# Kernel optimization log

Hardware: AMD Instinct MI355X
Metric: run time of the kernel (lower is better)

Reference implementation:

```python
import jax, jax.numpy as jnp
import numpy as np

B, T, I, H, N_LAYERS = 32, 1024, 512, 512, 4


def _custom_lstm(x, w, u, b):
    # x: [B,T,I]; w: [4,I,H] (gate order i,f,c,o); u: [4,H,H]; b: [4,H]
    # Preactivations for all timesteps/gates at once: [T,4,B,H]
    pre = jnp.einsum('bti,gih->tgbh', x, w) + b[None, :, None, :]
    h0 = jnp.zeros((x.shape[0], b.shape[-1]), x.dtype)
    c0 = jnp.zeros_like(h0)

    def step(carry, p):
        h, c = carry
        rec = jnp.einsum('bh,ghk->gbk', h, u)
        g = jax.nn.sigmoid(p + rec)          # all 4 gates use sigmoid (incl. g_t, as in source)
        i_t, f_t, g_t, o_t = g[0], g[1], g[2], g[3]
        c = f_t + c + i_t * g_t              # faithful: additive, not f*c
        h = o_t + jnp.tanh(c)                # faithful: additive, not o*tanh(c)
        return (h, c), h

    (h, c), hs = jax.lax.scan(step, (h0, c0), pre)
    return h, c, jnp.transpose(hs, (1, 0, 2))  # [B,T,H]


def _vlstm(x, h_prev, wx, wh, u, b):
    # x: [B,T,I]; h_prev: [B,T,H]; wx: [4,I,H]; wh: [4,H,H]; u: [4,H,H]; b: [4,H]
    # Source bug preserved: ALL gates use u[0] (u_i) and b[0] (b_i).
    pre = (jnp.einsum('bti,gih->tgbh', x, wx)
           + jnp.einsum('bth,ghk->tgbk', h_prev, wh)
           + b[0][None, None, None, :])
    u_i = u[0]
    h0 = jnp.zeros((x.shape[0], b.shape[-1]), x.dtype)
    c0 = jnp.zeros_like(h0)

    def step(carry, p):
        h, c = carry
        rec = h @ u_i                        # shared recurrent term for all gates
        g = jax.nn.sigmoid(p + rec[None])
        i_t, f_t, g_t, o_t = g[0], g[1], g[2], g[3]
        c = f_t + c + i_t * g_t
        h = o_t + jnp.tanh(c)
        return (h, c), h

    (h, c), hs = jax.lax.scan(step, (h0, c0), pre)
    return h, c, jnp.transpose(hs, (1, 0, 2))


def setup_inputs() -> dict:
    key = jax.random.key(0)
    ks = jax.random.split(key, 6)
    stdv = 1.0 / np.sqrt(H)
    u_ = lambda k, shp: jax.random.uniform(k, shp, jnp.float32, -stdv, stdv)
    L = N_LAYERS - 1
    return {
        'x': jax.random.normal(ks[0], (B, T, I), jnp.float32),
        'w1': u_(ks[1], (4, I, H)),
        'u1': u_(ks[2], (4, H, H)),
        'b1': u_(ks[3], (4, H)),
        'wx': u_(ks[4], (L, 4, I, H)),
        'wh': u_(ks[5], (L, 4, H, H)),
        'uv': u_(jax.random.fold_in(key, 10), (L, 4, H, H)),
        'bv': u_(jax.random.fold_in(key, 11), (L, 4, H)),
    }


def reference(x, w1, u1, b1, wx, wh, uv, bv):
    h_t, c_t, h_vec = _custom_lstm(x, w1, u1, b1)
    for l in range(wx.shape[0]):  # verbose path: each VLSTM sees raw x + prev layer h_vec
        h_t, c_t, h_vec = _vlstm(x, h_vec, wx[l], wh[l], uv[l], bv[l])
    return h_t, c_t, h_vec
```

## Files before the change

### kernel.cpp

```cpp
#include <hip/hip_runtime.h>

typedef unsigned short u16;
typedef unsigned int u32;
typedef unsigned long long u64;
typedef __attribute__((ext_vector_type(4))) float f32x4;
typedef __attribute__((ext_vector_type(8))) short short8;
typedef __attribute__((ext_vector_type(4))) short short4v;

__device__ __forceinline__ float bf2f(u16 v){ u32 b = ((u32)v)<<16; float f; __builtin_memcpy(&f,&b,4); return f; }
__device__ __forceinline__ u16 f2bf(float f){ u32 b; __builtin_memcpy(&b,&f,4); b = b + 0x7fffu + ((b>>16)&1u); return (u16)(b>>16); }
__device__ __forceinline__ float sigm(float x){ return 1.f/(1.f+__expf(-x)); }
__device__ __forceinline__ float tanh_a(float x){ return 1.f - 2.f/(__expf(2.f*x)+1.f); }
__device__ __forceinline__ int imin(int a, int b){ return a<b?a:b; }

typedef const __attribute__((address_space(1))) u32* gas1;
typedef __attribute__((address_space(3))) u32* las3;
__device__ __forceinline__ void gld16(const u16* g, u16* l){
  __builtin_amdgcn_global_load_lds((gas1)g, (las3)l, 16, 0, 0);
}

__device__ __forceinline__ void pub64(u32* p, u64 v){
  __hip_atomic_store((u64*)p, v, __ATOMIC_RELAXED, __HIP_MEMORY_SCOPE_AGENT);
}
__device__ __forceinline__ void pub32(u32* p, u32 v){
  __hip_atomic_store(p, v, __ATOMIC_RELAXED, __HIP_MEMORY_SCOPE_AGENT);
}
__device__ __forceinline__ u64 pol64(const u32* p){
  return __hip_atomic_load((const u64*)p, __ATOMIC_RELAXED, __HIP_MEMORY_SCOPE_AGENT);
}
__device__ __forceinline__ u32 pol32(const u32* p){
  return __hip_atomic_load(p, __ATOMIC_RELAXED, __HIP_MEMORY_SCOPE_AGENT);
}

__global__ void cast_x_kernel(const float* __restrict__ in, u16* __restrict__ out){
  int i = blockIdx.x*256 + threadIdx.x;
  for (; i < 4194304; i += 2048*256){
    f32x4 v = ((const f32x4*)in)[i];
    int e = i*4;
    int b = e >> 19, t = (e >> 9) & 1023, k = e & 511;
    short4v o;
    o[0]=(short)f2bf(v[0]); o[1]=(short)f2bf(v[1]); o[2]=(short)f2bf(v[2]); o[3]=(short)f2bf(v[3]);
    *(short4v*)&out[(size_t)(t*32+b)*512 + k] = o;
  }
}

__global__ void pack_w_kernel(const float* __restrict__ w1, const float* __restrict__ wx, const float* __restrict__ wh,
                              u16* __restrict__ w1p, u16* __restrict__ wxwhp){
  int e = blockIdx.x*256 + threadIdx.x;
  for (; e < 7340032; e += 2048*256){
    if (e < 1048576){
      int h = e & 511, k = (e>>9)&511, g = e>>18;
      w1p[(size_t)(g*512+h)*512 + k] = f2bf(w1[(size_t)g*262144 + (size_t)k*512 + h]);
    } else {
      int r = e - 1048576;
      int lv = r >> 21;
      int q = r & 2097151;
      int n = q >> 10, k = q & 1023;
      int g = n >> 9, h = n & 511;
      float v;
      if (k < 512) v = wx[(size_t)lv*1048576 + (size_t)g*262144 + (size_t)k*512 + h];
      else         v = wh[(size_t)lv*1048576 + (size_t)g*262144 + (size_t)(k-512)*512 + h];
      wxwhp[(size_t)lv*2097152 + (size_t)n*1024 + k] = f2bf(v);
    }
  }
}

__global__ void cast_u_kernel(const float* __restrict__ u1, const float* __restrict__ uv,
                              u16* __restrict__ u1p, u16* __restrict__ uv0p){
  int e = blockIdx.x*256 + threadIdx.x;
  for (; e < 1835008; e += 1024*256){
    if (e < 1048576) u1p[e] = f2bf(u1[e]);
    else { int r = e - 1048576; uv0p[r] = f2bf(uv[(size_t)(r>>18)*1048576 + (r & 262143)]); }
  }
}

__global__ __launch_bounds__(256) void gemm_pre_kernel(
    const u16* __restrict__ A1, const u16* __restrict__ B1,
    const float* __restrict__ bias, int bmask,
    u16* __restrict__ Out)
{
  __shared__ u16 As[128*64];
  __shared__ u16 Bs[128*64];
  const int tid = threadIdx.x;
  const int w = tid>>6, lane = tid&63;
  const int l15 = lane&15, l4 = lane>>4;
  const int m0 = blockIdx.x*128, n0 = blockIdx.y*128;
  const int wm = w>>1, wn = w&1;
  f32x4 acc[4][4];
#pragma unroll
  for (int a=0;a<4;a++)
#pragma unroll
    for (int bq=0;bq<4;bq++) acc[a][bq] = (f32x4){0.f,0.f,0.f,0.f};

  for (int kt=0;kt<8;kt++){
    const int k0 = kt*64;
    __syncthreads();
#pragma unroll
    for (int i=0;i<4;i++){
      int chunk = w*4 + i;
      int fb = chunk*1024 + lane*16;
      int row = fb>>7;
      int slot = (fb>>4)&7;
      const u16* srcA = A1 + (size_t)(m0+row)*512 + k0 + ((slot ^ (row&7))<<3);
      gld16(srcA, (u16*)As + chunk*512);
      const u16* srcB = B1 + (size_t)(n0+row)*512 + k0 + ((slot ^ (row&7))<<3);
      gld16(srcB, (u16*)Bs + chunk*512);
    }
    __syncthreads();
#pragma unroll
    for (int kk=0;kk<2;kk++){
      short8 af[4], bfq[4];
#pragma unroll
      for (int mi=0;mi<4;mi++){
        int row = wm*64 + mi*16 + l15;
        int s16 = l4 + kk*4;
        af[mi] = *(const short8*)&As[row*64 + ((s16 ^ (row&7))<<3)];
      }
#pragma unroll
      for (int ni=0;ni<4;ni++){
        int row = wn*64 + ni*16 + l15;
        int s16 = l4 + kk*4;
        bfq[ni] = *(const short8*)&Bs[row*64 + ((s16 ^ (row&7))<<3)];
      }
#pragma unroll
      for (int mi=0;mi<4;mi++)
#pragma unroll
        for (int ni=0;ni<4;ni++)
          acc[mi][ni] = __builtin_amdgcn_mfma_f32_16x16x32_bf16(af[mi], bfq[ni], acc[mi][ni], 0,0,0);
    }
  }
#pragma unroll
  for (int ni=0;ni<4;ni++){
    int col = n0 + wn*64 + ni*16 + l15;
    float bb = bias[col & bmask];
#pragma unroll
    for (int mi=0;mi<4;mi++){
#pragma unroll
      for (int i=0;i<4;i++){
        int row = m0 + wm*64 + mi*16 + l4*4 + i;
        Out[(size_t)row*2048 + col] = f2bf(acc[mi][ni][i] + bb);
      }
    }
  }
}

__global__ __launch_bounds__(512,2) void mega_kernel(
    const u16* __restrict__ pre1, const u16* __restrict__ u1p,
    const u16* __restrict__ uv0p, const u16* __restrict__ xb,
    const u16* __restrict__ wxwhp, const float* __restrict__ bv,
    u32* hring, u32* pring, u32* prog, float* __restrict__ out)
{
  __shared__ char smem[33024];
  const int bid = blockIdx.x;
  const int tid = threadIdx.x;
  const int lane = tid&63, w = tid>>6;
  const int l15 = lane&15, l4 = lane>>4;

  if (bid < 16){
    u16* hs = (u16*)smem;
    float* recb = (float*)(smem+16384);
    const int gk = bid & 7, gb = bid >> 3;
    const int b0 = gb*16, kb = gk*64;
    const int g = w>>1, ch = w&1;
    short8 bfr[2][16];
#pragma unroll
    for (int n=0;n<2;n++){
      const u16* up = u1p + (size_t)g*262144 + (kb + ch*32 + n*16 + l15);
#pragma unroll
      for (int s=0;s<16;s++){
        int kbase = s*32 + l4*8;
#pragma unroll
        for (int j=0;j<8;j++) bfr[n][s][j] = (short)up[(size_t)(kbase+j)*512];
      }
    }
    { short8 z = {0,0,0,0,0,0,0,0};
      for (int i=tid;i<1024;i+=512) ((short8*)hs)[i]=z; }
    const int b = tid>>5, q = tid&31;
    const int hc2 = q*2;
    float cA=0.f, cB=0.f;
    __syncthreads();

    for (int t=0;t<1024;++t){
      if ((t&15)==0 && t>=32){
        int thr = t-32;
        for(;;){
          int m0=(int)pol32(&prog[0]); m0=imin(m0,(int)pol32(&prog[1]));
          m0=imin(m0,(int)pol32(&prog[2])); m0=imin(m0,(int)pol32(&prog[3]));
          if (m0>=thr) break;
          __builtin_amdgcn_s_sleep(8);
        }
      }
      const u16* prow = pre1 + ((size_t)(t*32 + b0 + b))*2048 + kb + hc2;
      u32 pw0 = *(const u32*)(prow);
      u32 pw1 = *(const u32*)(prow+512);
      u32 pw2 = *(const u32*)(prow+1024);
      u32 pw3 = *(const u32*)(prow+1536);
      f32x4 acc0 = {0.f,0.f,0.f,0.f}, acc1 = {0.f,0.f,0.f,0.f};
      {
        int rb = l15*512, sw = (l15&7)<<3;
#pragma unroll
        for (int s=0;s<16;s++){
          short8 a = *(const short8*)&hs[rb + ((s*32 + l4*8) ^ sw)];
          acc0 = __builtin_amdgcn_mfma_f32_16x16x32_bf16(a, bfr[0][s], acc0, 0,0,0);
          acc1 = __builtin_amdgcn_mfma_f32_16x16x32_bf16(a, bfr[1][s], acc1, 0,0,0);
        }
      }
      {
        int base = g*64 + ch*32 + l15;
#pragma unroll
        for (int i=0;i<4;i++){
          recb[(l4*4+i)*256 + base]      = acc0[i];
          recb[(l4*4+i)*256 + base + 16] = acc1[i];
        }
      }
      __syncthreads();
      float ri0 = recb[b*256 + hc2],       ri1 = recb[b*256 + hc2+1];
      float rf0 = recb[b*256 + 64 + hc2],  rf1 = recb[b*256 + 64 + hc2+1];
      float rg0 = recb[b*256 + 128 + hc2], rg1 = recb[b*256 + 128 + hc2+1];
      float ro0 = recb[b*256 + 192 + hc2], ro1 = recb[b*256 + 192 + hc2+1];
      float gi0 = sigm(bf2f((u16)(pw0&0xffffu)) + ri0), gi1 = sigm(bf2f((u16)(pw0>>16)) + ri1);
      float gf0 = sigm(bf2f((u16)(pw1&0xffffu)) + rf0), gf1 = sigm(bf2f((u16)(pw1>>16)) + rf1);
      float gg0 = sigm(bf2f((u16)(pw2&0xffffu)) + rg0), gg1 = sigm(bf2f((u16)(pw2>>16)) + rg1);
      float go0 = sigm(bf2f((u16)(pw3&0xffffu)) + ro0), go1 = sigm(bf2f((u16)(pw3>>16)) + ro1);
      cA = gf0 + cA + gi0*gg0; float h0v = go0 + tanh_a(cA);
      cB = gf1 + cB + gi1*gg1; float h1v = go1 + tanh_a(cB);
      u16 hb0 = f2bf(h0v), hb1 = f2bf(h1v);
      const u32 tag = (u32)(t+1);
      u32* slot = hring + (size_t)(t&63)*16384;
      u64 msg = (((u64)((tag<<16)|(u32)hb1))<<32) | (u64)((tag<<16)|(u32)hb0);
      pub64(&slot[(size_t)(b0+b)*512 + kb + hc2], msg);
      u32 hpair = (u32)hb0 | ((u32)hb1<<16);
      *(u32*)&hs[b*512 + ((kb+hc2) ^ ((b&7)<<3))] = hpair;
      {
        const u32* srcg = slot + (size_t)(b0+b)*512;
        u64 nv[7];
        for(;;){
#pragma unroll
          for (int j=0;j<7;j++){
            int fc = q*14 + 2*j;
            int ac = fc + (fc>=kb ? 64 : 0);
            nv[j] = pol64(&srcg[ac]);
          }
          u32 ok = 1;
#pragma unroll
          for (int j=0;j<7;j++){
            if ((u32)(((u32)nv[j])>>16) != tag) ok=0;
            if ((u32)(nv[j]>>48) != tag) ok=0;
          }
          if (ok) break;
          __builtin_amdgcn_s_sleep(1);
        }
#pragma unroll
        for (int j=0;j<7;j++){
          int fc = q*14 + 2*j;
          int ac = fc + (fc>=kb ? 64 : 0);
          u32 pair = ((u32)nv[j]&0xffffu) | ((u32)((nv[j]>>32)&0xffffu)<<16);
          *(u32*)&hs[b*512 + (ac ^ ((b&7)<<3))] = pair;
        }
      }
      __syncthreads();
      if (tid==0) pub32(&prog[32+bid], (u32)(t+1));
    }
  } else if (bid < 28){
    u16* hs = (u16*)smem;
    float* recb = (float*)(smem+16384);
    const int l = 1 + ((bid-16)>>2);
    const int lv = l-1;
    const int sub = (bid-16)&3;
    const int ch = sub&1, gb = sub>>1;
    const int b0 = gb*16, cbase = ch*256;
    short8 bfr[2][16];
#pragma unroll
    for (int n=0;n<2;n++){
      const u16* up = uv0p + (size_t)lv*262144 + (cbase + w*32 + n*16 + l15);
#pragma unroll
      for (int s=0;s<16;s++){
        int kbase = s*32 + l4*8;
#pragma unroll
        for (int j=0;j<8;j++) bfr[n][s][j] = (short)up[(size_t)(kbase+j)*512];
      }
    }
    { short8 z = {0,0,0,0,0,0,0,0};
      for (int i=tid;i<1024;i+=512) ((short8*)hs)[i]=z; }
    const int b = tid>>5, q = tid&31;
    const int oc = cbase + q*8;
    float cv[8];
#pragma unroll
    for (int j=0;j<8;j++) cv[j]=0.f;
    u32* hr = hring + (size_t)l*1048576;
    u32* pr = pring + (size_t)lv*4194304;
    const int is_last = (l==3);
    __syncthreads();

    for (int t=0;t<1024;++t){
      const u32 tag = (u32)(t+1);
      if (l<3 && (t&15)==0 && t>=32){
        int thr=t-32;
        const int pbase = l*4;
        for(;;){
          int m0=(int)pol32(&prog[pbase]); m0=imin(m0,(int)pol32(&prog[pbase+1]));
          m0=imin(m0,(int)pol32(&prog[pbase+2])); m0=imin(m0,(int)pol32(&prog[pbase+3]));
          if (m0>=thr) break;
          __builtin_amdgcn_s_sleep(8);
        }
      }
      const u32* ps = pr + (size_t)(t&63)*65536 + (size_t)(b0+b)*2048;
      u64 pv[16];
#pragma unroll
      for (int gq=0;gq<4;gq++)
#pragma unroll
        for (int j=0;j<4;j++)
          pv[gq*4+j] = pol64(&ps[gq*512 + oc + 2*j]);
      f32x4 acc0={0.f,0.f,0.f,0.f}, acc1={0.f,0.f,0.f,0.f};
      {
        int rb=l15*512, sw=(l15&7)<<3;
#pragma unroll
        for (int s=0;s<16;s++){
          short8 a = *(const short8*)&hs[rb + ((s*32+l4*8)^sw)];
          acc0 = __builtin_amdgcn_mfma_f32_16x16x32_bf16(a, bfr[0][s], acc0, 0,0,0);
          acc1 = __builtin_amdgcn_mfma_f32_16x16x32_bf16(a, bfr[1][s], acc1, 0,0,0);
        }
      }
      {
        int base = w*32 + l15;
#pragma unroll
        for (int i=0;i<4;i++){
          recb[(l4*4+i)*256 + base]    = acc0[i];
          recb[(l4*4+i)*256 + base+16] = acc1[i];
        }
      }
      for(;;){
        u32 ok=1;
#pragma unroll
        for (int i=0;i<16;i++){
          if ((u32)(((u32)pv[i])>>16) != tag) ok=0;
          if ((u32)(pv[i]>>48) != tag) ok=0;
        }
        if (ok) break;
        for(;;){
          int mn = 0x7fffffff;
#pragma unroll
          for (int g=0; g<4; g++){
            int cg0 = g*4 + ch*2;
            mn = imin(mn, (int)pol32(&prog[64 + lv*32 + (cg0*2+gb)]));
            mn = imin(mn, (int)pol32(&prog[64 + lv*32 + ((cg0+1)*2+gb)]));
          }
          if (mn >= (int)tag) break;
          __builtin_amdgcn_s_sleep(4);
        }
#pragma unroll
        for (int gq=0;gq<4;gq++)
#pragma unroll
          for (int j=0;j<4;j++)
            pv[gq*4+j] = pol64(&ps[gq*512 + oc + 2*j]);
      }
      __syncthreads();
      short8 hvv; float hf[8]; u32 msgw[8];
#pragma unroll
      for (int j=0;j<8;j++){
        float r = recb[b*256 + q*8 + j];
        int wi = j>>1;
        u32 w0 = (j&1) ? (u32)(pv[wi]>>32)    : (u32)pv[wi];
        u32 w1v= (j&1) ? (u32)(pv[4+wi]>>32)  : (u32)pv[4+wi];
        u32 w2 = (j&1) ? (u32)(pv[8+wi]>>32)  : (u32)pv[8+wi];
        u32 w3 = (j&1) ? (u32)(pv[12+wi]>>32) : (u32)pv[12+wi];
        float gi = sigm(bf2f((u16)(w0&0xffffu)) + r);
        float gf = sigm(bf2f((u16)(w1v&0xffffu)) + r);
        float gg = sigm(bf2f((u16)(w2&0xffffu)) + r);
        float go = sigm(bf2f((u16)(w3&0xffffu)) + r);
        cv[j] = gf + cv[j] + gi*gg;
        float h = go + tanh_a(cv[j]);
        u16 hb = f2bf(h);
        hvv[j]=(short)hb; hf[j]=h; msgw[j] = (tag<<16)|(u32)hb;
      }
      u32* hslot = hr + (size_t)(t&63)*16384 + (size_t)(b0+b)*512;
#pragma unroll
      for (int j=0;j<4;j++){
        u64 m = (((u64)msgw[2*j+1])<<32) | (u64)msgw[2*j];
        pub64(&hslot[oc + 2*j], m);
      }
      *(short8*)&hs[b*512 + (oc ^ ((b&7)<<3))] = hvv;
      if (is_last){
        f32x4 h4a={hf[0],hf[1],hf[2],hf[3]}, h4b={hf[4],hf[5],hf[6],hf[7]};
        *(f32x4*)&out[32768 + ((size_t)((b0+b)*1024+t))*512 + oc]   = h4a;
        *(f32x4*)&out[32768 + ((size_t)((b0+b)*1024+t))*512 + oc+4] = h4b;
        if (t==1023){
          *(f32x4*)&out[(size_t)(b0+b)*512 + oc]   = h4a;
          *(f32x4*)&out[(size_t)(b0+b)*512 + oc+4] = h4b;
          f32x4 c4a={cv[0],cv[1],cv[2],cv[3]}, c4b={cv[4],cv[5],cv[6],cv[7]};
          *(f32x4*)&out[16384 + (size_t)(b0+b)*512 + oc]   = c4a;
          *(f32x4*)&out[16384 + (size_t)(b0+b)*512 + oc+4] = c4b;
        }
      }
      {
        const u32* src = hslot + (ch^1)*256 + q*8;
        u64 nv[4];
        for(;;){
#pragma unroll
          for (int j=0;j<4;j++) nv[j] = pol64(&src[2*j]);
          u32 ok=1;
#pragma unroll
          for (int j=0;j<4;j++){
            if ((u32)(((u32)nv[j])>>16)!=tag) ok=0;
            if ((u32)(nv[j]>>48)!=tag) ok=0;
          }
          if (ok) break;
          __builtin_amdgcn_s_sleep(1);
        }
        short8 hh;
#pragma unroll
        for (int j=0;j<4;j++){
          hh[2*j]   = (short)(u16)(nv[j] & 0xffffu);
          hh[2*j+1] = (short)(u16)((nv[j]>>32) & 0xffffu);
        }
        int pc = (ch^1)*256 + q*8;
        *(short8*)&hs[b*512 + (pc ^ ((b&7)<<3))] = hh;
      }
      __syncthreads();
      if (tid==0) pub32(&prog[(l-1)*4 + sub], (u32)(t+1));
    }
  } else {
    u16* hstage = (u16*)smem;
    const int idx = bid - 28;
    const int lv = idx >> 5;
    const int r  = idx & 31;
    const int gb = r & 1, cg = r >> 1;
    const int b0 = gb*16;
    const int c  = cg*128 + w*16 + l15;
    const u16* Bw = wxwhp + (size_t)lv*2097152 + (size_t)c*1024;
    short8 bfr[32];
#pragma unroll
    for (int s=0;s<32;s++) bfr[s] = *(const short8*)&Bw[s*32 + l4*8];
    const float bias = bv[lv*2048 + (c & 511)];
    const int prow_ = tid >> 5;
    const int px = tid & 31;
    const u32* hrb = hring + (size_t)lv*1048576;
    u32* prb = pring + (size_t)lv*4194304;

    for (int t=0;t<1024;++t){
      const u32 tag = (u32)(t+1);
      const u32* hsrc = hrb + (size_t)(t&63)*16384 + (size_t)(b0+prow_)*512;
      u64 nv[8];
#pragma unroll
      for (int j=0;j<8;j++) nv[j] = pol64(&hsrc[px*2 + 64*j]);
      f32x4 acc = {0.f,0.f,0.f,0.f};
      const u16* xrow = xb + (size_t)(t*32 + b0 + l15)*512;
#pragma unroll
      for (int s=0;s<16;s++){
        short8 a = *(const short8*)&xrow[s*32 + l4*8];
        acc = __builtin_amdgcn_mfma_f32_16x16x32_bf16(a, bfr[s], acc, 0,0,0);
      }
      for(;;){
        u32 ok=1;
#pragma unroll
        for (int j=0;j<8;j++){
          if ((u32)(((u32)nv[j])>>16)!=tag) ok=0;
          if ((u32)(nv[j]>>48)!=tag) ok=0;
        }
        if (ok) break;
        if (lv==0){
          for(;;){
            int mn = 0x7fffffff;
#pragma unroll
            for (int j=0;j<8;j++) mn = imin(mn, (int)pol32(&prog[32 + gb*8 + j]));
            if (mn >= (int)tag) break;
            __builtin_amdgcn_s_sleep(4);
          }
        } else {
          for(;;){
            int a2 = (int)pol32(&prog[(lv-1)*4 + gb*2]);
            int c2 = (int)pol32(&prog[(lv-1)*4 + gb*2 + 1]);
            if (imin(a2,c2) >= (int)tag) break;
            __builtin_amdgcn_s_sleep(4);
          }
        }
#pragma unroll
        for (int j=0;j<8;j++) nv[j] = pol64(&hsrc[px*2 + 64*j]);
      }
#pragma unroll
      for (int j=0;j<8;j++){
        u32 pair = ((u32)nv[j]&0xffffu) | ((u32)((nv[j]>>32)&0xffffu)<<16);
        *(u32*)&hstage[prow_*520 + px*2 + 64*j] = pair;
      }
      __syncthreads();
#pragma unroll
      for (int s=0;s<16;s++){
        short8 a = *(const short8*)&hstage[l15*520 + s*32 + l4*8];
        acc = __builtin_amdgcn_mfma_f32_16x16x32_bf16(a, bfr[16+s], acc, 0,0,0);
      }
      u32* dst = prb + (size_t)(t&63)*65536 + c;
#pragma unroll
      for (int i=0;i<4;i++){
        u32 v = ((u32)f2bf(acc[i]+bias)) | (tag<<16);
        pub32(&dst[(size_t)(b0 + l4*4 + i)*2048], v);
      }
      __syncthreads();
      if (tid==0) pub32(&prog[64 + lv*32 + r], (u32)(t+1));
    }
  }
}

extern "C" void kernel_launch(void* const* d_in, const int* in_sizes, int n_in,
                              void* d_out, int out_size, void* d_ws, size_t ws_size,
                              hipStream_t stream)
{
  const float* x  = (const float*)d_in[0];
  const float* w1 = (const float*)d_in[1];
  const float* u1 = (const float*)d_in[2];
  const float* b1 = (const float*)d_in[3];
  const float* wx = (const float*)d_in[4];
  const float* wh = (const float*)d_in[5];
  const float* uv = (const float*)d_in[6];
  const float* bv = (const float*)d_in[7];
  float* out = (float*)d_out;

  char* p = (char*)d_ws;
  u16* pre1  = (u16*)p; p += (size_t)134217728;
  u16* xb    = (u16*)p; p += 33554432;
  u16* w1p   = (u16*)p; p += 2097152;
  u16* wxwhp = (u16*)p; p += 12582912;
  u16* u1p   = (u16*)p; p += 2097152;
  u16* uv0p  = (u16*)p; p += 1572864;
  u32* hring = (u32*)p; p += 16777216;
  u32* pring = (u32*)p; p += 50331648;
  u32* prog  = (u32*)p; p += 1024;
  if ((size_t)(p - (char*)d_ws) > ws_size) return;

  hipMemsetAsync(hring, 0, 16777216, stream);
  hipMemsetAsync(pring, 0, 50331648, stream);
  hipMemsetAsync(prog, 0, 1024, stream);
  cast_x_kernel<<<2048,256,0,stream>>>(x, xb);
  pack_w_kernel<<<2048,256,0,stream>>>(w1, wx, wh, w1p, wxwhp);
  cast_u_kernel<<<1024,256,0,stream>>>(u1, uv, u1p, uv0p);

  gemm_pre_kernel<<<dim3(256,16),256,0,stream>>>(xb, w1p, b1, 2047, pre1);
  mega_kernel<<<124,512,0,stream>>>(pre1, u1p, uv0p, xb, wxwhp, bv, hring, pring, prog, out);
}
```

Before: 7.624 ms.

## Repartition persistent LSTM mega-kernel to full-batch blocks with XCD-aware role mapping

Each persistent block in the wavefront-pipelined LSTM kernel now handles all 32 batch rows instead of 16. Recurrent blocks run two M-tiles of MFMA per step, which halves the number of blocks that must exchange h each timestep. Block roles are assigned by bid&7, so each layer's cooperating blocks presumably sit on the same XCD. Per-element tag polling is replaced by a few threads spinning on progress counters followed by a lightweight barrier. The change trades per-block work and register pressure (larger pv and nv arrays) for fewer cross-block synchronisations and better cache locality, and it adds idle early-exit blocks.

```diff
diff --git a/kernel.cpp b/kernel.cpp
--- a/kernel.cpp
+++ b/kernel.cpp
@@ -11,7 +11,6 @@
 __device__ __forceinline__ u16 f2bf(float f){ u32 b; __builtin_memcpy(&b,&f,4); b = b + 0x7fffu + ((b>>16)&1u); return (u16)(b>>16); }
 __device__ __forceinline__ float sigm(float x){ return 1.f/(1.f+__expf(-x)); }
 __device__ __forceinline__ float tanh_a(float x){ return 1.f - 2.f/(__expf(2.f*x)+1.f); }
-__device__ __forceinline__ int imin(int a, int b){ return a<b?a:b; }
 
 typedef const __attribute__((address_space(1))) u32* gas1;
 typedef __attribute__((address_space(3))) u32* las3;
@@ -30,6 +29,12 @@
 }
 __device__ __forceinline__ u32 pol32(const u32* p){
   return __hip_atomic_load(p, __ATOMIC_RELAXED, __HIP_MEMORY_SCOPE_AGENT);
+}
+
+__device__ __forceinline__ void barx(){
+  asm volatile("s_waitcnt lgkmcnt(0)" ::: "memory");
+  __builtin_amdgcn_s_barrier();
+  __builtin_amdgcn_sched_barrier(0);
 }
 
 __global__ void cast_x_kernel(const float* __restrict__ in, u16* __restrict__ out){
@@ -82,10 +87,10 @@
   __shared__ u16 As[128*64];
   __shared__ u16 Bs[128*64];
   const int tid = threadIdx.x;
-  const int w = tid>>6, lane = tid&63;
+  const int wv = tid>>6, lane = tid&63;
   const int l15 = lane&15, l4 = lane>>4;
   const int m0 = blockIdx.x*128, n0 = blockIdx.y*128;
-  const int wm = w>>1, wn = w&1;
+  const int wm = wv>>1, wn = wv&1;
   f32x4 acc[4][4];
 #pragma unroll
   for (int a=0;a<4;a++)
@@ -97,7 +102,7 @@
     __syncthreads();
 #pragma unroll
     for (int i=0;i<4;i++){
-      int chunk = w*4 + i;
+      int chunk = wv*4 + i;
       int fb = chunk*1024 + lane*16;
       int row = fb>>7;
       int slot = (fb>>4)&7;
@@ -150,18 +155,19 @@
     const u16* __restrict__ wxwhp, const float* __restrict__ bv,
     u32* hring, u32* pring, u32* prog, float* __restrict__ out)
 {
-  __shared__ char smem[33024];
+  __shared__ char smem[66560];
   const int bid = blockIdx.x;
+  const int x = bid & 7, rr_ = bid >> 3;
   const int tid = threadIdx.x;
-  const int lane = tid&63, w = tid>>6;
+  const int lane = tid&63, wv = tid>>6;
   const int l15 = lane&15, l4 = lane>>4;
 
-  if (bid < 16){
+  if (x == 0){
+    if (rr_ >= 8) return;
     u16* hs = (u16*)smem;
-    float* recb = (float*)(smem+16384);
-    const int gk = bid & 7, gb = bid >> 3;
-    const int b0 = gb*16, kb = gk*64;
-    const int g = w>>1, ch = w&1;
+    float* recb = (float*)(smem+32768);
+    const int gk = rr_, kb = gk*64;
+    const int g = wv>>1, ch = wv&1;
     short8 bfr[2][16];
 #pragma unroll
     for (int n=0;n<2;n++){
@@ -174,76 +180,80 @@
       }
     }
     { short8 z = {0,0,0,0,0,0,0,0};
-      for (int i=tid;i<1024;i+=512) ((short8*)hs)[i]=z; }
-    const int b = tid>>5, q = tid&31;
-    const int hc2 = q*2;
-    float cA=0.f, cB=0.f;
+      for (int i=tid;i<2048;i+=512) ((short8*)hs)[i]=z; }
+    const int b = tid>>4, q = tid&15;
+    const int c0 = q*4;
+    float cc[4] = {0.f,0.f,0.f,0.f};
     __syncthreads();
 
     for (int t=0;t<1024;++t){
-      if ((t&15)==0 && t>=32){
-        int thr = t-32;
-        for(;;){
-          int m0=(int)pol32(&prog[0]); m0=imin(m0,(int)pol32(&prog[1]));
-          m0=imin(m0,(int)pol32(&prog[2])); m0=imin(m0,(int)pol32(&prog[3]));
-          if (m0>=thr) break;
-          __builtin_amdgcn_s_sleep(8);
-        }
-      }
-      const u16* prow = pre1 + ((size_t)(t*32 + b0 + b))*2048 + kb + hc2;
-      u32 pw0 = *(const u32*)(prow);
-      u32 pw1 = *(const u32*)(prow+512);
-      u32 pw2 = *(const u32*)(prow+1024);
-      u32 pw3 = *(const u32*)(prow+1536);
-      f32x4 acc0 = {0.f,0.f,0.f,0.f}, acc1 = {0.f,0.f,0.f,0.f};
-      {
-        int rb = l15*512, sw = (l15&7)<<3;
+      const u32 tag = (u32)(t+1);
+      if ((t&15)==0 && t>=48){
+        int thr = t-48;
+        if (tid<16){ while ((int)pol32(&prog[16+tid]) < thr) __builtin_amdgcn_s_sleep(8); }
+        barx();
+      }
+      const u16* prow = pre1 + (size_t)(t*32 + b)*2048 + kb + c0;
+      u64 pw0 = *(const u64*)(prow);
+      u64 pw1 = *(const u64*)(prow+512);
+      u64 pw2 = *(const u64*)(prow+1024);
+      u64 pw3 = *(const u64*)(prow+1536);
+      f32x4 acc[2][2];
+#pragma unroll
+      for (int m=0;m<2;m++){ acc[m][0]=(f32x4){0,0,0,0}; acc[m][1]=(f32x4){0,0,0,0}; }
+#pragma unroll
+      for (int m=0;m<2;m++){
+        int rb = (m*16+l15)*512, sw = (l15&7)<<3;
 #pragma unroll
         for (int s=0;s<16;s++){
           short8 a = *(const short8*)&hs[rb + ((s*32 + l4*8) ^ sw)];
-          acc0 = __builtin_amdgcn_mfma_f32_16x16x32_bf16(a, bfr[0][s], acc0, 0,0,0);
-          acc1 = __builtin_amdgcn_mfma_f32_16x16x32_bf16(a, bfr[1][s], acc1, 0,0,0);
+          acc[m][0] = __builtin_amdgcn_mfma_f32_16x16x32_bf16(a, bfr[0][s], acc[m][0], 0,0,0);
+          acc[m][1] = __builtin_amdgcn_mfma_f32_16x16x32_bf16(a, bfr[1][s], acc[m][1], 0,0,0);
         }
       }
       {
         int base = g*64 + ch*32 + l15;
 #pragma unroll
-        for (int i=0;i<4;i++){
-          recb[(l4*4+i)*256 + base]      = acc0[i];
-          recb[(l4*4+i)*256 + base + 16] = acc1[i];
-        }
-      }
-      __syncthreads();
-      float ri0 = recb[b*256 + hc2],       ri1 = recb[b*256 + hc2+1];
-      float rf0 = recb[b*256 + 64 + hc2],  rf1 = recb[b*256 + 64 + hc2+1];
-      float rg0 = recb[b*256 + 128 + hc2], rg1 = recb[b*256 + 128 + hc2+1];
-      float ro0 = recb[b*256 + 192 + hc2], ro1 = recb[b*256 + 192 + hc2+1];
-      float gi0 = sigm(bf2f((u16)(pw0&0xffffu)) + ri0), gi1 = sigm(bf2f((u16)(pw0>>16)) + ri1);
-      float gf0 = sigm(bf2f((u16)(pw1&0xffffu)) + rf0), gf1 = sigm(bf2f((u16)(pw1>>16)) + rf1);
-      float gg0 = sigm(bf2f((u16)(pw2&0xffffu)) + rg0), gg1 = sigm(bf2f((u16)(pw2>>16)) + rg1);
-      float go0 = sigm(bf2f((u16)(pw3&0xffffu)) + ro0), go1 = sigm(bf2f((u16)(pw3>>16)) + ro1);
-      cA = gf0 + cA + gi0*gg0; float h0v = go0 + tanh_a(cA);
-      cB = gf1 + cB + gi1*gg1; float h1v = go1 + tanh_a(cB);
-      u16 hb0 = f2bf(h0v), hb1 = f2bf(h1v);
-      const u32 tag = (u32)(t+1);
-      u32* slot = hring + (size_t)(t&63)*16384;
-      u64 msg = (((u64)((tag<<16)|(u32)hb1))<<32) | (u64)((tag<<16)|(u32)hb0);
-      pub64(&slot[(size_t)(b0+b)*512 + kb + hc2], msg);
-      u32 hpair = (u32)hb0 | ((u32)hb1<<16);
-      *(u32*)&hs[b*512 + ((kb+hc2) ^ ((b&7)<<3))] = hpair;
+        for (int m=0;m<2;m++)
+#pragma unroll
+          for (int n=0;n<2;n++)
+#pragma unroll
+            for (int i=0;i<4;i++)
+              recb[(m*16 + l4*4 + i)*256 + base + n*16] = acc[m][n][i];
+      }
+      barx();
+      u16 hb[4];
+#pragma unroll
+      for (int j=0;j<4;j++){
+        float ri = recb[b*256 + c0 + j];
+        float rf = recb[b*256 + 64 + c0 + j];
+        float rg = recb[b*256 + 128 + c0 + j];
+        float ro = recb[b*256 + 192 + c0 + j];
+        float gi = sigm(bf2f((u16)(pw0>>(16*j))) + ri);
+        float gf = sigm(bf2f((u16)(pw1>>(16*j))) + rf);
+        float gg = sigm(bf2f((u16)(pw2>>(16*j))) + rg);
+        float go = sigm(bf2f((u16)(pw3>>(16*j))) + ro);
+        cc[j] = gf + cc[j] + gi*gg;
+        hb[j] = f2bf(go + tanh_a(cc[j]));
+      }
+      u32* slot = hring + (size_t)(t&63)*16384 + (size_t)b*512;
+      pub64(&slot[kb+c0],   (((u64)((tag<<16)|(u32)hb[1]))<<32) | (u64)((tag<<16)|(u32)hb[0]));
+      pub64(&slot[kb+c0+2], (((u64)((tag<<16)|(u32)hb[3]))<<32) | (u64)((tag<<16)|(u32)hb[2]));
+      const int swb = (b&7)<<3;
+      *(u32*)&hs[b*512 + ((kb+c0)   ^ swb)] = (u32)hb[0] | ((u32)hb[1]<<16);
+      *(u32*)&hs[b*512 + ((kb+c0+2) ^ swb)] = (u32)hb[2] | ((u32)hb[3]<<16);
       {
-        const u32* srcg = slot + (size_t)(b0+b)*512;
-        u64 nv[7];
+        u64 nv[14];
         for(;;){
 #pragma unroll
-          for (int j=0;j<7;j++){
-            int fc = q*14 + 2*j;
+          for (int j=0;j<14;j++){
+            int fc = q*28 + 2*j;
             int ac = fc + (fc>=kb ? 64 : 0);
-            nv[j] = pol64(&srcg[ac]);
+            nv[j] = pol64(&slot[ac]);
           }
           u32 ok = 1;
 #pragma unroll
-          for (int j=0;j<7;j++){
+          for (int j=0;j<14;j++){
             if ((u32)(((u32)nv[j])>>16) != tag) ok=0;
             if ((u32)(nv[j]>>48) != tag) ok=0;
           }
@@ -251,28 +261,25 @@
           __builtin_amdgcn_s_sleep(1);
         }
 #pragma unroll
-        for (int j=0;j<7;j++){
-          int fc = q*14 + 2*j;
+        for (int j=0;j<14;j++){
+          int fc = q*28 + 2*j;
           int ac = fc + (fc>=kb ? 64 : 0);
-          u32 pair = ((u32)nv[j]&0xffffu) | ((u32)((nv[j]>>32)&0xffffu)<<16);
-          *(u32*)&hs[b*512 + (ac ^ ((b&7)<<3))] = pair;
-        }
-      }
-      __syncthreads();
-      if (tid==0) pub32(&prog[32+bid], (u32)(t+1));
-    }
-  } else if (bid < 28){
+          *(u32*)&hs[b*512 + (ac ^ swb)] = ((u32)nv[j]&0xffffu) | (((u32)(nv[j]>>32)&0xffffu)<<16);
+        }
+      }
+      barx();
+      if (tid==0) pub32(&prog[gk], tag);
+    }
+  } else if (x <= 3){
+    if (rr_ >= 2) return;
     u16* hs = (u16*)smem;
-    float* recb = (float*)(smem+16384);
-    const int l = 1 + ((bid-16)>>2);
-    const int lv = l-1;
-    const int sub = (bid-16)&3;
-    const int ch = sub&1, gb = sub>>1;
-    const int b0 = gb*16, cbase = ch*256;
+    float* recb = (float*)(smem+32768);
+    const int l = x, lv = l-1, ch = rr_;
+    const int cbase = ch*256;
     short8 bfr[2][16];
 #pragma unroll
     for (int n=0;n<2;n++){
-      const u16* up = uv0p + (size_t)lv*262144 + (cbase + w*32 + n*16 + l15);
+      const u16* up = uv0p + (size_t)lv*262144 + (cbase + wv*32 + n*16 + l15);
 #pragma unroll
       for (int s=0;s<16;s++){
         int kbase = s*32 + l4*8;
@@ -281,12 +288,12 @@
       }
     }
     { short8 z = {0,0,0,0,0,0,0,0};
-      for (int i=tid;i<1024;i+=512) ((short8*)hs)[i]=z; }
-    const int b = tid>>5, q = tid&31;
-    const int oc = cbase + q*8;
-    float cv[8];
-#pragma unroll
-    for (int j=0;j<8;j++) cv[j]=0.f;
+      for (int i=tid;i<2048;i+=512) ((short8*)hs)[i]=z; }
+    const int b = tid>>4, q = tid&15;
+    const int oc = cbase + q*16;
+    float cv[16];
+#pragma unroll
+    for (int j=0;j<16;j++) cv[j]=0.f;
     u32* hr = hring + (size_t)l*1048576;
     u32* pr = pring + (size_t)lv*4194304;
     const int is_last = (l==3);
@@ -294,208 +301,213 @@
 
     for (int t=0;t<1024;++t){
       const u32 tag = (u32)(t+1);
-      if (l<3 && (t&15)==0 && t>=32){
-        int thr=t-32;
-        const int pbase = l*4;
-        for(;;){
-          int m0=(int)pol32(&prog[pbase]); m0=imin(m0,(int)pol32(&prog[pbase+1]));
-          m0=imin(m0,(int)pol32(&prog[pbase+2])); m0=imin(m0,(int)pol32(&prog[pbase+3]));
-          if (m0>=thr) break;
-          __builtin_amdgcn_s_sleep(8);
-        }
-      }
-      const u32* ps = pr + (size_t)(t&63)*65536 + (size_t)(b0+b)*2048;
-      u64 pv[16];
-#pragma unroll
-      for (int gq=0;gq<4;gq++)
-#pragma unroll
-        for (int j=0;j<4;j++)
-          pv[gq*4+j] = pol64(&ps[gq*512 + oc + 2*j]);
-      f32x4 acc0={0.f,0.f,0.f,0.f}, acc1={0.f,0.f,0.f,0.f};
+      if (l<3 && (t&15)==0 && t>=48){
+        int thr = t-48;
+        if (tid<16){ while ((int)pol32(&prog[16 + l*16 + tid]) < thr) __builtin_amdgcn_s_sleep(8); }
+        barx();
+      }
+      if (tid<16){ while ((int)pol32(&prog[16 + lv*16 + tid]) < (int)tag) __builtin_amdgcn_s_sleep(8); }
+      barx();
+      const u32* ps = pr + (size_t)(t&63)*65536 + (size_t)b*2048;
+      u64 pv[32];
+#pragma unroll
+      for (int g4=0;g4<4;g4++)
+#pragma unroll
+        for (int j=0;j<8;j++)
+          pv[g4*8+j] = pol64(&ps[g4*512 + oc + 2*j]);
+      f32x4 acc[2][2];
+#pragma unroll
+      for (int m=0;m<2;m++){ acc[m][0]=(f32x4){0,0,0,0}; acc[m][1]=(f32x4){0,0,0,0}; }
+#pragma unroll
+      for (int m=0;m<2;m++){
+        int rb = (m*16+l15)*512, sw = (l15&7)<<3;
+#pragma unroll
+        for (int s=0;s<16;s++){
+          short8 a = *(const short8*)&hs[rb + ((s*32 + l4*8) ^ sw)];
+          acc[m][0] = __builtin_amdgcn_mfma_f32_16x16x32_bf16(a, bfr[0][s], acc[m][0], 0,0,0);
+          acc[m][1] = __builtin_amdgcn_mfma_f32_16x16x32_bf16(a, bfr[1][s], acc[m][1], 0,0,0);
+        }
+      }
       {
-        int rb=l15*512, sw=(l15&7)<<3;
-#pragma unroll
-        for (int s=0;s<16;s++){
-          short8 a = *(const short8*)&hs[rb + ((s*32+l4*8)^sw)];
-          acc0 = __builtin_amdgcn_mfma_f32_16x16x32_bf16(a, bfr[0][s], acc0, 0,0,0);
-          acc1 = __builtin_amdgcn_mfma_f32_16x16x32_bf16(a, bfr[1][s], acc1, 0,0,0);
-        }
-      }
-      {
-        int base = w*32 + l15;
-#pragma unroll
-        for (int i=0;i<4;i++){
-          recb[(l4*4+i)*256 + base]    = acc0[i];
-          recb[(l4*4+i)*256 + base+16] = acc1[i];
-        }
+        int base = wv*32 + l15;
+#pragma unroll
+        for (int m=0;m<2;m++)
+#pragma unroll
+          for (int n=0;n<2;n++)
+#pragma unroll
+            for (int i=0;i<4;i++)
+              recb[(m*16 + l4*4 + i)*256 + base + n*16] = acc[m][n][i];
       }
       for(;;){
         u32 ok=1;
 #pragma unroll
-        for (int i=0;i<16;i++){
+        for (int i=0;i<32;i++){
           if ((u32)(((u32)pv[i])>>16) != tag) ok=0;
           if ((u32)(pv[i]>>48) != tag) ok=0;
         }
         if (ok) break;
-        for(;;){
-          int mn = 0x7fffffff;
-#pragma unroll
-          for (int g=0; g<4; g++){
-            int cg0 = g*4 + ch*2;
-            mn = imin(mn, (int)pol32(&prog[64 + lv*32 + (cg0*2+gb)]));
-            mn = imin(mn, (int)pol32(&prog[64 + lv*32 + ((cg0+1)*2+gb)]));
-          }
-          if (mn >= (int)tag) break;
-          __builtin_amdgcn_s_sleep(4);
-        }
-#pragma unroll
-        for (int gq=0;gq<4;gq++)
-#pragma unroll
-          for (int j=0;j<4;j++)
-            pv[gq*4+j] = pol64(&ps[gq*512 + oc + 2*j]);
-      }
-      __syncthreads();
-      short8 hvv; float hf[8]; u32 msgw[8];
-#pragma unroll
-      for (int j=0;j<8;j++){
-        float r = recb[b*256 + q*8 + j];
-        int wi = j>>1;
-        u32 w0 = (j&1) ? (u32)(pv[wi]>>32)    : (u32)pv[wi];
-        u32 w1v= (j&1) ? (u32)(pv[4+wi]>>32)  : (u32)pv[4+wi];
-        u32 w2 = (j&1) ? (u32)(pv[8+wi]>>32)  : (u32)pv[8+wi];
-        u32 w3 = (j&1) ? (u32)(pv[12+wi]>>32) : (u32)pv[12+wi];
-        float gi = sigm(bf2f((u16)(w0&0xffffu)) + r);
-        float gf = sigm(bf2f((u16)(w1v&0xffffu)) + r);
-        float gg = sigm(bf2f((u16)(w2&0xffffu)) + r);
-        float go = sigm(bf2f((u16)(w3&0xffffu)) + r);
+        __builtin_amdgcn_s_sleep(2);
+#pragma unroll
+        for (int g4=0;g4<4;g4++)
+#pragma unroll
+          for (int j=0;j<8;j++)
+            pv[g4*8+j] = pol64(&ps[g4*512 + oc + 2*j]);
+      }
+      barx();
+      u16 hb[16]; float hf[16];
+#pragma unroll
+      for (int j=0;j<16;j++){
+        float rv = recb[b*256 + q*16 + j];
+        u32 w0 = (u32)(pv[(j>>1)]      >> (32*(j&1)));
+        u32 w1v= (u32)(pv[8+(j>>1)]    >> (32*(j&1)));
+        u32 w2 = (u32)(pv[16+(j>>1)]   >> (32*(j&1)));
+        u32 w3 = (u32)(pv[24+(j>>1)]   >> (32*(j&1)));
+        float gi = sigm(bf2f((u16)w0) + rv);
+        float gf = sigm(bf2f((u16)w1v) + rv);
+        float gg = sigm(bf2f((u16)w2) + rv);
+        float go = sigm(bf2f((u16)w3) + rv);
         cv[j] = gf + cv[j] + gi*gg;
         float h = go + tanh_a(cv[j]);
-        u16 hb = f2bf(h);
-        hvv[j]=(short)hb; hf[j]=h; msgw[j] = (tag<<16)|(u32)hb;
-      }
-      u32* hslot = hr + (size_t)(t&63)*16384 + (size_t)(b0+b)*512;
-#pragma unroll
-      for (int j=0;j<4;j++){
-        u64 m = (((u64)msgw[2*j+1])<<32) | (u64)msgw[2*j];
-        pub64(&hslot[oc + 2*j], m);
-      }
-      *(short8*)&hs[b*512 + (oc ^ ((b&7)<<3))] = hvv;
+        hb[j] = f2bf(h); hf[j] = h;
+      }
+      u32* hslot = hr + (size_t)(t&63)*16384 + (size_t)b*512;
+#pragma unroll
+      for (int jj=0;jj<8;jj++){
+        u64 m = (((u64)((tag<<16)|(u32)hb[2*jj+1]))<<32) | (u64)((tag<<16)|(u32)hb[2*jj]);
+        pub64(&hslot[oc + 2*jj], m);
+      }
+      const int swb = (b&7)<<3;
+#pragma unroll
+      for (int jh=0;jh<2;jh++){
+        short8 hv8;
+#pragma unroll
+        for (int i=0;i<8;i++) hv8[i] = (short)hb[jh*8+i];
+        *(short8*)&hs[b*512 + ((oc + jh*8) ^ swb)] = hv8;
+      }
       if (is_last){
-        f32x4 h4a={hf[0],hf[1],hf[2],hf[3]}, h4b={hf[4],hf[5],hf[6],hf[7]};
-        *(f32x4*)&out[32768 + ((size_t)((b0+b)*1024+t))*512 + oc]   = h4a;
-        *(f32x4*)&out[32768 + ((size_t)((b0+b)*1024+t))*512 + oc+4] = h4b;
+#pragma unroll
+        for (int jq=0;jq<4;jq++){
+          f32x4 h4 = {hf[jq*4],hf[jq*4+1],hf[jq*4+2],hf[jq*4+3]};
+          *(f32x4*)&out[32768 + ((size_t)(b*1024+t))*512 + oc + jq*4] = h4;
+        }
         if (t==1023){
-          *(f32x4*)&out[(size_t)(b0+b)*512 + oc]   = h4a;
-          *(f32x4*)&out[(size_t)(b0+b)*512 + oc+4] = h4b;
-          f32x4 c4a={cv[0],cv[1],cv[2],cv[3]}, c4b={cv[4],cv[5],cv[6],cv[7]};
-          *(f32x4*)&out[16384 + (size_t)(b0+b)*512 + oc]   = c4a;
-          *(f32x4*)&out[16384 + (size_t)(b0+b)*512 + oc+4] = c4b;
+#pragma unroll
+          for (int jq=0;jq<4;jq++){
+            f32x4 h4 = {hf[jq*4],hf[jq*4+1],hf[jq*4+2],hf[jq*4+3]};
+            f32x4 c4 = {cv[jq*4],cv[jq*4+1],cv[jq*4+2],cv[jq*4+3]};
+            *(f32x4*)&out[(size_t)b*512 + oc + jq*4] = h4;
+            *(f32x4*)&out[16384 + (size_t)b*512 + oc + jq*4] = c4;
+          }
         }
       }
       {
-        const u32* src = hslot + (ch^1)*256 + q*8;
-        u64 nv[4];
+        const int pc = (ch^1)*256 + q*16;
+        const u32* src = hslot + pc;
+        u64 nv[8];
         for(;;){
 #pragma unroll
-          for (int j=0;j<4;j++) nv[j] = pol64(&src[2*j]);
+          for (int j=0;j<8;j++) nv[j] = pol64(&src[2*j]);
           u32 ok=1;
 #pragma unroll
-          for (int j=0;j<4;j++){
+          for (int j=0;j<8;j++){
             if ((u32)(((u32)nv[j])>>16)!=tag) ok=0;
             if ((u32)(nv[j]>>48)!=tag) ok=0;
           }
           if (ok) break;
           __builtin_amdgcn_s_sleep(1);
         }
-        short8 hh;
-#pragma unroll
-        for (int j=0;j<4;j++){
-          hh[2*j]   = (short)(u16)(nv[j] & 0xffffu);
-          hh[2*j+1] = (short)(u16)((nv[j]>>32) & 0xffffu);
-        }
-        int pc = (ch^1)*256 + q*8;
-        *(short8*)&hs[b*512 + (pc ^ ((b&7)<<3))] = hh;
-      }
-      __syncthreads();
-      if (tid==0) pub32(&prog[(l-1)*4 + sub], (u32)(t+1));
-    }
-  } else {
+#pragma unroll
+        for (int jh=0;jh<2;jh++){
+          short8 hh;
+#pragma unroll
+          for (int i=0;i<4;i++){
+            hh[2*i]   = (short)(u16)(nv[jh*4+i] & 0xffffu);
+            hh[2*i+1] = (short)(u16)((nv[jh*4+i]>>32) & 0xffffu);
+          }
+          *(short8*)&hs[b*512 + ((pc + jh*8) ^ swb)] = hh;
+        }
+      }
+      barx();
+      if (tid==0) pub32(&prog[8 + lv*2 + ch], tag);
+    }
+  } else if (x <= 6){
+    if (rr_ >= 16) return;
     u16* hstage = (u16*)smem;
-    const int idx = bid - 28;
-    const int lv = idx >> 5;
-    const int r  = idx & 31;
-    const int gb = r & 1, cg = r >> 1;
-    const int b0 = gb*16;
-    const int c  = cg*128 + w*16 + l15;
+    const int lv = x-4, cg = rr_;
+    const int c = cg*128 + wv*16 + l15;
     const u16* Bw = wxwhp + (size_t)lv*2097152 + (size_t)c*1024;
     short8 bfr[32];
 #pragma unroll
     for (int s=0;s<32;s++) bfr[s] = *(const short8*)&Bw[s*32 + l4*8];
     const float bias = bv[lv*2048 + (c & 511)];
-    const int prow_ = tid >> 5;
-    const int px = tid & 31;
+    const int pb = tid>>4, pq = tid&15;
     const u32* hrb = hring + (size_t)lv*1048576;
     u32* prb = pring + (size_t)lv*4194304;
 
     for (int t=0;t<1024;++t){
       const u32 tag = (u32)(t+1);
-      const u32* hsrc = hrb + (size_t)(t&63)*16384 + (size_t)(b0+prow_)*512;
-      u64 nv[8];
-#pragma unroll
-      for (int j=0;j<8;j++) nv[j] = pol64(&hsrc[px*2 + 64*j]);
-      f32x4 acc = {0.f,0.f,0.f,0.f};
-      const u16* xrow = xb + (size_t)(t*32 + b0 + l15)*512;
-#pragma unroll
-      for (int s=0;s<16;s++){
-        short8 a = *(const short8*)&xrow[s*32 + l4*8];
-        acc = __builtin_amdgcn_mfma_f32_16x16x32_bf16(a, bfr[s], acc, 0,0,0);
+      if ((t&15)==0 && t>=48){
+        int thr = t-48;
+        if (tid<2){ while ((int)pol32(&prog[8 + lv*2 + tid]) < thr) __builtin_amdgcn_s_sleep(8); }
+        barx();
+      }
+      if (lv==0){
+        if (tid<8){ while ((int)pol32(&prog[tid]) < (int)tag) __builtin_amdgcn_s_sleep(8); }
+      } else {
+        if (tid<2){ while ((int)pol32(&prog[8 + (lv-1)*2 + tid]) < (int)tag) __builtin_amdgcn_s_sleep(8); }
+      }
+      barx();
+      const u32* hsrc = hrb + (size_t)(t&63)*16384 + (size_t)pb*512 + pq*32;
+      u64 nv[16];
+#pragma unroll
+      for (int j=0;j<16;j++) nv[j] = pol64(&hsrc[2*j]);
+      f32x4 acc[2] = {(f32x4){0,0,0,0},(f32x4){0,0,0,0}};
+#pragma unroll
+      for (int m=0;m<2;m++){
+        const u16* xrow = xb + (size_t)(t*32 + m*16 + l15)*512;
+#pragma unroll
+        for (int s=0;s<16;s++){
+          short8 a = *(const short8*)&xrow[s*32 + l4*8];
+          acc[m] = __builtin_amdgcn_mfma_f32_16x16x32_bf16(a, bfr[s], acc[m], 0,0,0);
+        }
       }
       for(;;){
         u32 ok=1;
 #pragma unroll
-        for (int j=0;j<8;j++){
+        for (int j=0;j<16;j++){
           if ((u32)(((u32)nv[j])>>16)!=tag) ok=0;
           if ((u32)(nv[j]>>48)!=tag) ok=0;
         }
         if (ok) break;
-        if (lv==0){
-          for(;;){
-            int mn = 0x7fffffff;
-#pragma unroll
-            for (int j=0;j<8;j++) mn = imin(mn, (int)pol32(&prog[32 + gb*8 + j]));
-            if (mn >= (int)tag) break;
-            __builtin_amdgcn_s_sleep(4);
-          }
-        } else {
-          for(;;){
-            int a2 = (int)pol32(&prog[(lv-1)*4 + gb*2]);
-            int c2 = (int)pol32(&prog[(lv-1)*4 + gb*2 + 1]);
-            if (imin(a2,c2) >= (int)tag) break;
-            __builtin_amdgcn_s_sleep(4);
-          }
-        }
-#pragma unroll
-        for (int j=0;j<8;j++) nv[j] = pol64(&hsrc[px*2 + 64*j]);
-      }
-#pragma unroll
-      for (int j=0;j<8;j++){
-        u32 pair = ((u32)nv[j]&0xffffu) | ((u32)((nv[j]>>32)&0xffffu)<<16);
-        *(u32*)&hstage[prow_*520 + px*2 + 64*j] = pair;
-      }
-      __syncthreads();
-#pragma unroll
-      for (int s=0;s<16;s++){
-        short8 a = *(const short8*)&hstage[l15*520 + s*32 + l4*8];
-        acc = __builtin_amdgcn_mfma_f32_16x16x32_bf16(a, bfr[16+s], acc, 0,0,0);
+        __builtin_amdgcn_s_sleep(2);
+#pragma unroll
+        for (int j=0;j<16;j++) nv[j] = pol64(&hsrc[2*j]);
+      }
+#pragma unroll
+      for (int j=0;j<16;j++){
+        u32 pair = ((u32)nv[j]&0xffffu) | (((u32)(nv[j]>>32)&0xffffu)<<16);
+        *(u32*)&hstage[pb*520 + pq*32 + 2*j] = pair;
+      }
+      barx();
+#pragma unroll
+      for (int m=0;m<2;m++){
+        int arow = (m*16+l15)*520;
+#pragma unroll
+        for (int s=0;s<16;s++){
+          short8 a = *(const short8*)&hstage[arow + s*32 + l4*8];
+          acc[m] = __builtin_amdgcn_mfma_f32_16x16x32_bf16(a, bfr[16+s], acc[m], 0,0,0);
+        }
       }
       u32* dst = prb + (size_t)(t&63)*65536 + c;
 #pragma unroll
-      for (int i=0;i<4;i++){
-        u32 v = ((u32)f2bf(acc[i]+bias)) | (tag<<16);
-        pub32(&dst[(size_t)(b0 + l4*4 + i)*2048], v);
-      }
-      __syncthreads();
-      if (tid==0) pub32(&prog[64 + lv*32 + r], (u32)(t+1));
+      for (int m=0;m<2;m++)
+#pragma unroll
+        for (int i=0;i<4;i++){
+          u32 v = ((u32)f2bf(acc[m][i]+bias)) | (tag<<16);
+          pub32(&dst[(size_t)(m*16 + l4*4 + i)*2048], v);
+        }
+      barx();
+      if (tid==0) pub32(&prog[16 + lv*16 + cg], tag);
     }
   }
 }
@@ -534,5 +546,5 @@
   cast_u_kernel<<<1024,256,0,stream>>>(u1, uv, u1p, uv0p);
 
   gemm_pre_kernel<<<dim3(256,16),256,0,stream>>>(xb, w1p, b1, 2047, pre1);
-  mega_kernel<<<124,512,0,stream>>>(pre1, u1p, uv0p, xb, wxwhp, bv, hring, pring, prog, out);
-}
+  mega_kernel<<<128,512,0,stream>>>(pre1, u1p, uv0p, xb, wxwhp, bv, hring, pring, prog, out);
+}
```

Measured after the change: 24.93 ms. 3.27x slower.
